# Kernel optimization log

Measured on AMD Instinct MI355X. Metric: run time of the kernel, lower is better.

## Reference

```python
import jax, jax.numpy as jnp
import numpy as np

N_NODES = 100000
N_EDGES = 1600000


def setup_inputs() -> dict:
    key = jax.random.key(0)
    ks = jax.random.split(key, 6)
    x = jax.random.normal(ks[0], (N_NODES, 128), dtype=jnp.float32)
    src = jax.random.randint(ks[1], (N_EDGES,), 0, N_NODES, dtype=jnp.int32)
    dst = jax.random.randint(ks[2], (N_EDGES,), 0, N_NODES, dtype=jnp.int32)
    # Glorot-ish scaled weights
    W1 = jax.random.normal(ks[3], (128, 64), dtype=jnp.float32) / np.sqrt(128.0)
    b1 = jnp.zeros((64,), dtype=jnp.float32)
    W2 = jax.random.normal(ks[4], (64, 64), dtype=jnp.float32) / np.sqrt(64.0)
    b2 = jnp.zeros((64,), dtype=jnp.float32)
    return {"x": x, "src": src, "dst": dst, "W1": W1, "b1": b1, "W2": W2, "b2": b2}


def _gcn_forward(x, src_f, dst_f, norm_src, norm_dst, W1, b1, W2, b2):
    n = x.shape[0]

    def conv(h, W, b):
        # weight-first (in_feats >= out_feats in DGL GraphConv): h W is cheap, aggregate small dim
        h = h @ W                                  # [N, d_out]
        h = h * norm_src[:, None]                  # D_out^{-1/2} on source side
        msg = h[src_f]                             # gather per edge [E+N, d_out]
        agg = jax.ops.segment_sum(msg, dst_f, num_segments=n)  # scatter-add to dst
        return agg * norm_dst[:, None] + b         # D_in^{-1/2} + bias

    h = jax.nn.relu(conv(x, W1, b1))
    return conv(h, W2, b2)


def reference(x, src, dst, W1, b1, W2, b2):
    n = x.shape[0]
    loop = jnp.arange(n, dtype=src.dtype)
    src_f = jnp.concatenate([src, loop])  # dgl.add_self_loop
    dst_f = jnp.concatenate([dst, loop])
    ones = jnp.ones(src_f.shape[0], dtype=x.dtype)
    out_deg = jax.ops.segment_sum(ones, src_f, num_segments=n)
    in_deg = jax.ops.segment_sum(ones, dst_f, num_segments=n)
    norm_src = jax.lax.rsqrt(out_deg)  # deg >= 1 due to self loops
    norm_dst = jax.lax.rsqrt(in_deg)
    return _gcn_forward(x, src_f, dst_f, norm_src, norm_dst, W1, b1, W2, b2)
```

## Files before the change

### kernel.cpp

```cpp
#include <hip/hip_runtime.h>
#include <hip/hip_fp16.h>

#define D 64
#define SLICE 33400
#define NBUCK 512
#define EPB 4096

typedef __attribute__((ext_vector_type(8))) short short8;
typedef __attribute__((ext_vector_type(4))) float floatx4;

__global__ __launch_bounds__(1024) void k_hist(const int* __restrict__ src,
                                               const int* __restrict__ dst,
                                               int* __restrict__ cnt_out,
                                               int* __restrict__ cnt_in,
                                               int E, int N) {
    __shared__ int h[SLICE];
    const int* idx = blockIdx.z ? dst : src;
    int* cnt       = blockIdx.z ? cnt_in : cnt_out;
    int lo = blockIdx.y * SLICE;
    int hi = min(lo + SLICE, N);
    int len = hi - lo;
    for (int i = threadIdx.x; i < len; i += 1024) h[i] = 0;
    __syncthreads();

    const int E4 = E >> 2;
    const int4* idx4 = (const int4*)idx;
    int stride = gridDim.x * 1024;
    for (int i = blockIdx.x * 1024 + threadIdx.x; i < E4; i += stride) {
        int4 v = idx4[i];
        if (v.x >= lo && v.x < hi) atomicAdd(&h[v.x - lo], 1);
        if (v.y >= lo && v.y < hi) atomicAdd(&h[v.y - lo], 1);
        if (v.z >= lo && v.z < hi) atomicAdd(&h[v.z - lo], 1);
        if (v.w >= lo && v.w < hi) atomicAdd(&h[v.w - lo], 1);
    }
    if (blockIdx.x == 0) {
        int e = E4 * 4 + threadIdx.x;
        if (e < E) {
            int v = idx[e];
            if (v >= lo && v < hi) atomicAdd(&h[v - lo], 1);
        }
    }
    __syncthreads();
    for (int i = threadIdx.x; i < len; i += 1024) {
        int c = h[i];
        if (c) atomicAdd(&cnt[lo + i], c);
    }
}

__global__ __launch_bounds__(256) void k_norm(const int* __restrict__ cnt,
                                              float* __restrict__ nrm, int n) {
    int i = blockIdx.x * 256 + threadIdx.x;
    if (i < n) nrm[i] = rsqrtf((float)cnt[i] + 1.0f);
}

__global__ __launch_bounds__(256) void k_scan1(const int* __restrict__ in,
                                               int* __restrict__ out,
                                               int* __restrict__ partials, int n) {
    __shared__ int s[256];
    int tid = threadIdx.x;
    int base = blockIdx.x * 1024 + tid * 4;
    int v[4];
#pragma unroll
    for (int j = 0; j < 4; ++j) v[j] = (base + j < n) ? in[base + j] : 0;
    int l1 = v[0] + v[1];
    int l2 = l1 + v[2];
    int total = l2 + v[3];
    s[tid] = total;
    __syncthreads();
    for (int off = 1; off < 256; off <<= 1) {
        int add = (tid >= off) ? s[tid - off] : 0;
        __syncthreads();
        s[tid] += add;
        __syncthreads();
    }
    int excl = s[tid] - total;
    if (base + 0 < n) out[base + 0] = excl;
    if (base + 1 < n) out[base + 1] = excl + v[0];
    if (base + 2 < n) out[base + 2] = excl + l1;
    if (base + 3 < n) out[base + 3] = excl + l2;
    if (tid == 255) partials[blockIdx.x] = s[255];
}

__global__ __launch_bounds__(256) void k_scan2(int* __restrict__ partials, int B,
                                               int* __restrict__ row_ptr, int N, int E) {
    __shared__ int s[256];
    int tid = threadIdx.x;
    int v = (tid < B) ? partials[tid] : 0;
    s[tid] = v;
    __syncthreads();
    for (int off = 1; off < 256; off <<= 1) {
        int add = (tid >= off) ? s[tid - off] : 0;
        __syncthreads();
        s[tid] += add;
        __syncthreads();
    }
    if (tid < B) partials[tid] = s[tid] - v;
    if (tid == 0) row_ptr[N] = E;
}

__global__ __launch_bounds__(256) void k_scan3(int* __restrict__ out,
                                               const int* __restrict__ partials, int n) {
    int off = partials[blockIdx.x];
    int base = blockIdx.x * 1024 + threadIdx.x * 4;
#pragma unroll
    for (int j = 0; j < 4; ++j)
        if (base + j < n) out[base + j] += off;
}

__global__ __launch_bounds__(256) void k_bin(const int* __restrict__ src,
                                             const int* __restrict__ dst,
                                             const int* __restrict__ row_ptr,
                                             int* __restrict__ bucket_cursor,
                                             unsigned long long* __restrict__ binned,
                                             int E) {
    __shared__ int cnt[NBUCK];
    __shared__ int bloc[NBUCK];
    __shared__ int lcur[NBUCK];
    __shared__ int gbase[NBUCK];
    __shared__ int ss[256];
    __shared__ unsigned long long stage[EPB];

    int tid = threadIdx.x;
    int start = blockIdx.x * EPB;
    int nloc = min(EPB, E - start);

    for (int i = tid; i < NBUCK; i += 256) cnt[i] = 0;
    __syncthreads();

#pragma unroll
    for (int r = 0; r < EPB / 256; ++r) {
        int idx = start + r * 256 + tid;
        if (idx < E) atomicAdd(&cnt[dst[idx] >> 8], 1);
    }
    __syncthreads();

    int a = cnt[2 * tid], b = cnt[2 * tid + 1];
    ss[tid] = a + b;
    __syncthreads();
    for (int off = 1; off < 256; off <<= 1) {
        int add = (tid >= off) ? ss[tid - off] : 0;
        __syncthreads();
        ss[tid] += add;
        __syncthreads();
    }
    int excl = ss[tid] - (a + b);
    bloc[2 * tid] = excl;           lcur[2 * tid] = excl;
    bloc[2 * tid + 1] = excl + a;   lcur[2 * tid + 1] = excl + a;
    __syncthreads();

    for (int bk = tid; bk < NBUCK; bk += 256) {
        int c = cnt[bk];
        gbase[bk] = c ? (atomicAdd(&bucket_cursor[bk], c) + row_ptr[bk << 8]) : 0;
    }
    __syncthreads();

#pragma unroll
    for (int r = 0; r < EPB / 256; ++r) {
        int idx = start + r * 256 + tid;
        if (idx < E) {
            int d = dst[idx];
            int p = atomicAdd(&lcur[d >> 8], 1);
            stage[p] = ((unsigned long long)(unsigned)d << 32) | (unsigned)src[idx];
        }
    }
    __syncthreads();

#pragma unroll
    for (int r = 0; r < EPB / 256; ++r) {
        int i = r * 256 + tid;
        if (i < nloc) {
            unsigned long long e = stage[i];
            int bk = (int)(e >> 40);
            binned[gbase[bk] + (i - bloc[bk])] = e;
        }
    }
}

__global__ __launch_bounds__(256) void k_bsort(const unsigned long long* __restrict__ binned,
                                               const int* __restrict__ row_ptr,
                                               int* __restrict__ csr, int N) {
    __shared__ int cur[256];
    int b = blockIdx.x;
    int n0 = b << 8;
    int tid = threadIdx.x;
    if (n0 + tid < N) cur[tid] = row_ptr[n0 + tid];
    __syncthreads();
    int base = row_ptr[n0];
    int c = row_ptr[min(n0 + 256, N)] - base;
    for (int k = tid; k < c; k += 256) {
        unsigned long long e = binned[base + k];
        int d = (int)(e >> 32);
        int s = (int)(e & 0xffffffffu);
        int p = atomicAdd(&cur[d - n0], 1);
        csr[p] = s;
    }
}

template <int K>
__global__ __launch_bounds__(256) void k_gemm_mfma(const float* __restrict__ hsrc,
                                                   const float* __restrict__ W,
                                                   const float* __restrict__ norm_src,
                                                   __half* __restrict__ t, int N) {
    constexpr int NKI = K / 32;
    __shared__ short Whi[NKI * 2048];
    __shared__ short Wlo[NKI * 2048];
    int tid = threadIdx.x;

    for (int f = tid; f < K * 64; f += 256) {
        int n  = f & 15;
        int j  = (f >> 4) & 7;
        int q  = (f >> 7) & 3;
        int ct = (f >> 9) & 3;
        int ki = f >> 11;
        int k = ki * 32 + q * 8 + j;
        int c = ct * 16 + n;
        float w = W[k * 64 + c];
        unsigned u = __float_as_uint(w);
        float l = w - __uint_as_float(u & 0xffff0000u);
        int idx = (((ki * 4 + ct) * 16 + n) * 4 + q) * 8 + j;
        Whi[idx] = (short)(u >> 16);
        Wlo[idx] = (short)(__float_as_uint(l) >> 16);
    }
    __syncthreads();

    int wave = tid >> 6, lane = tid & 63;
    int q = lane >> 4, n = lane & 15;
    int r0 = blockIdx.x * 64 + wave * 16;
    int rowc = min(r0 + n, N - 1);

    floatx4 acc[4] = {{0.f,0.f,0.f,0.f},{0.f,0.f,0.f,0.f},
                      {0.f,0.f,0.f,0.f},{0.f,0.f,0.f,0.f}};

    for (int ki = 0; ki < NKI; ++ki) {
        const float* ap = hsrc + (long long)rowc * K + ki * 32 + q * 8;
        float4 a0 = *(const float4*)ap;
        float4 a1 = *(const float4*)(ap + 4);
        float av[8] = {a0.x, a0.y, a0.z, a0.w, a1.x, a1.y, a1.z, a1.w};
        short8 ahi, alo;
#pragma unroll
        for (int j = 0; j < 8; ++j) {
            unsigned u = __float_as_uint(av[j]);
            float l = av[j] - __uint_as_float(u & 0xffff0000u);
            ahi[j] = (short)(u >> 16);
            alo[j] = (short)(__float_as_uint(l) >> 16);
        }
#pragma unroll
        for (int ct = 0; ct < 4; ++ct) {
            int bidx = (((ki * 4 + ct) * 16 + n) * 4 + q) * 8;
            short8 bhi = *(const short8*)&Whi[bidx];
            short8 blo = *(const short8*)&Wlo[bidx];
            acc[ct] = __builtin_amdgcn_mfma_f32_16x16x32_bf16(ahi, bhi, acc[ct], 0, 0, 0);
            acc[ct] = __builtin_amdgcn_mfma_f32_16x16x32_bf16(ahi, blo, acc[ct], 0, 0, 0);
            acc[ct] = __builtin_amdgcn_mfma_f32_16x16x32_bf16(alo, bhi, acc[ct], 0, 0, 0);
        }
    }

#pragma unroll
    for (int reg = 0; reg < 4; ++reg) {
        int orow = r0 + q * 4 + reg;
        if (orow < N) {
            float nrm = norm_src[orow];
#pragma unroll
            for (int ct = 0; ct < 4; ++ct)
                t[(long long)orow * 64 + ct * 16 + n] = __float2half(acc[ct][reg] * nrm);
        }
    }
}

__global__ __launch_bounds__(256) void k_agg(const int* __restrict__ row_ptr,
                                             const int* __restrict__ cnt,
                                             const int* __restrict__ csr,
                                             const __half* __restrict__ t,
                                             const float* __restrict__ norm_dst,
                                             const float* __restrict__ bias,
                                             float* __restrict__ out, int N, int do_relu) {
    int tid = threadIdx.x;
    int half_id = tid >> 5;
    int lane = tid & 31;
    int i = blockIdx.x * 8 + half_id;
    if (i >= N) return;
    const __half2* t2 = (const __half2*)t;
    int start = row_ptr[i], c = cnt[i];

    float2 sf = __half22float2(t2[i * 32 + lane]);
    float ax = sf.x, ay = sf.y;

    int j = 0;
    int pre = min(c, (4 - (start & 3)) & 3);
    for (; j < pre; ++j) {
        float2 f = __half22float2(t2[csr[start + j] * 32 + lane]);
        ax += f.x; ay += f.y;
    }
    for (; j + 8 <= c; j += 8) {
        int4 s4 = *(const int4*)&csr[start + j];
        int4 s5 = *(const int4*)&csr[start + j + 4];
        float2 f0 = __half22float2(t2[s4.x * 32 + lane]);
        float2 f1 = __half22float2(t2[s4.y * 32 + lane]);
        float2 f2 = __half22float2(t2[s4.z * 32 + lane]);
        float2 f3 = __half22float2(t2[s4.w * 32 + lane]);
        float2 f4 = __half22float2(t2[s5.x * 32 + lane]);
        float2 f5 = __half22float2(t2[s5.y * 32 + lane]);
        float2 f6 = __half22float2(t2[s5.z * 32 + lane]);
        float2 f7 = __half22float2(t2[s5.w * 32 + lane]);
        ax += ((f0.x + f1.x) + (f2.x + f3.x)) + ((f4.x + f5.x) + (f6.x + f7.x));
        ay += ((f0.y + f1.y) + (f2.y + f3.y)) + ((f4.y + f5.y) + (f6.y + f7.y));
    }
    for (; j + 4 <= c; j += 4) {
        int4 s4 = *(const int4*)&csr[start + j];
        float2 f0 = __half22float2(t2[s4.x * 32 + lane]);
        float2 f1 = __half22float2(t2[s4.y * 32 + lane]);
        float2 f2 = __half22float2(t2[s4.z * 32 + lane]);
        float2 f3 = __half22float2(t2[s4.w * 32 + lane]);
        ax += (f0.x + f1.x) + (f2.x + f3.x);
        ay += (f0.y + f1.y) + (f2.y + f3.y);
    }
    for (; j < c; ++j) {
        float2 f = __half22float2(t2[csr[start + j] * 32 + lane]);
        ax += f.x; ay += f.y;
    }

    float nrm = norm_dst[i];
    float2 bb = ((const float2*)bias)[lane];
    float vx = fmaf(ax, nrm, bb.x);
    float vy = fmaf(ay, nrm, bb.y);
    if (do_relu) { vx = fmaxf(vx, 0.f); vy = fmaxf(vy, 0.f); }
    float2 o; o.x = vx; o.y = vy;
    ((float2*)out)[i * 32 + lane] = o;
}

extern "C" void kernel_launch(void* const* d_in, const int* in_sizes, int n_in,
                              void* d_out, int out_size, void* d_ws, size_t ws_size,
                              hipStream_t stream) {
    const float* x   = (const float*)d_in[0];
    const int*   src = (const int*)d_in[1];
    const int*   dst = (const int*)d_in[2];
    const float* W1  = (const float*)d_in[3];
    const float* b1  = (const float*)d_in[4];
    const float* W2  = (const float*)d_in[5];
    const float* b2  = (const float*)d_in[6];
    float* out = (float*)d_out;

    const int N = in_sizes[0] / 128;
    const int E = in_sizes[1];

    int*   cnt_out  = (int*)d_ws;
    int*   cnt_in   = cnt_out + N;
    int*   row_ptr  = cnt_in + N;
    int*   partials = row_ptr + N + 1;
    float* norm_src = (float*)(partials + 1024);
    float* norm_dst = norm_src + N;
    long long toff = (5LL * N + 1025 + 63) & ~63LL;
    float* tbase    = (float*)d_ws + toff;
    float* h        = tbase + (long long)N * D;
    int*   csr      = (int*)(h + (long long)N * D);
    int*   bucket_cursor = csr + E;
    __half* t_h = (__half*)tbase;
    unsigned long long* binned = (unsigned long long*)tbase;

    const int B = (N + 1023) / 1024;
    const int NS = (N + SLICE - 1) / SLICE;
    const int NB = (N + 255) / 256;
    const int NBK = (E + EPB - 1) / EPB;

    hipMemsetAsync(cnt_out, 0, (size_t)2 * N * sizeof(int), stream);
    hipMemsetAsync(bucket_cursor, 0, (size_t)NBUCK * sizeof(int), stream);

    k_hist<<<dim3(42, NS, 2), 1024, 0, stream>>>(src, dst, cnt_out, cnt_in, E, N);
    k_norm<<<(2 * N + 255) / 256, 256, 0, stream>>>(cnt_out, norm_src, 2 * N);

    k_scan1<<<B, 256, 0, stream>>>(cnt_in, row_ptr, partials, N);
    k_scan2<<<1, 256, 0, stream>>>(partials, B, row_ptr, N, E);
    k_scan3<<<B, 256, 0, stream>>>(row_ptr, partials, N);

    k_bin<<<NBK, 256, 0, stream>>>(src, dst, row_ptr, bucket_cursor, binned, E);
    k_bsort<<<NB, 256, 0, stream>>>(binned, row_ptr, csr, N);

    k_gemm_mfma<128><<<(N + 63) / 64, 256, 0, stream>>>(x, W1, norm_src, t_h, N);
    k_agg<<<(N + 7) / 8, 256, 0, stream>>>(row_ptr, cnt_in, csr, t_h, norm_dst, b1, h, N, 1);

    k_gemm_mfma<64><<<(N + 63) / 64, 256, 0, stream>>>(h, W2, norm_src, t_h, N);
    k_agg<<<(N + 7) / 8, 256, 0, stream>>>(row_ptr, cnt_in, csr, t_h, norm_dst, b2, out, N, 0);
}
```

Baseline: 303.8 us.

## Derive CSR row pointers per bucket inside bsort instead of global in-degree scan

The per-node in-degree histogram and the three-kernel global scan are replaced by a 512-entry coarse bucket histogram folded into k_hist and a single-block bucket scan. Each k_bsort block now counts its own destination nodes, scans them locally, and writes row_ptr and both normalisation vectors, which removes k_norm and two scan kernels. This cuts kernel launches and a full pass over dst at node granularity, in exchange for an extra read of the binned edges inside k_bsort. k_agg now derives the degree from row_ptr differences.

```diff
diff --git a/kernel.cpp b/kernel.cpp
--- a/kernel.cpp
+++ b/kernel.cpp
@@ -12,22 +12,44 @@
 __global__ __launch_bounds__(1024) void k_hist(const int* __restrict__ src,
                                                const int* __restrict__ dst,
                                                int* __restrict__ cnt_out,
-                                               int* __restrict__ cnt_in,
+                                               int* __restrict__ bucket_cnt,
                                                int E, int N) {
     __shared__ int h[SLICE];
-    const int* idx = blockIdx.z ? dst : src;
-    int* cnt       = blockIdx.z ? cnt_in : cnt_out;
+    const int E4 = E >> 2;
+    int stride = gridDim.x * 1024;
+
+    if (blockIdx.y == gridDim.y - 1) {
+        for (int i = threadIdx.x; i < NBUCK; i += 1024) h[i] = 0;
+        __syncthreads();
+        const int4* d4 = (const int4*)dst;
+        for (int i = blockIdx.x * 1024 + threadIdx.x; i < E4; i += stride) {
+            int4 v = d4[i];
+            atomicAdd(&h[v.x >> 8], 1);
+            atomicAdd(&h[v.y >> 8], 1);
+            atomicAdd(&h[v.z >> 8], 1);
+            atomicAdd(&h[v.w >> 8], 1);
+        }
+        if (blockIdx.x == 0) {
+            int e = E4 * 4 + threadIdx.x;
+            if (e < E) atomicAdd(&h[dst[e] >> 8], 1);
+        }
+        __syncthreads();
+        for (int i = threadIdx.x; i < NBUCK; i += 1024) {
+            int c = h[i];
+            if (c) atomicAdd(&bucket_cnt[i], c);
+        }
+        return;
+    }
+
     int lo = blockIdx.y * SLICE;
     int hi = min(lo + SLICE, N);
     int len = hi - lo;
     for (int i = threadIdx.x; i < len; i += 1024) h[i] = 0;
     __syncthreads();
 
-    const int E4 = E >> 2;
-    const int4* idx4 = (const int4*)idx;
-    int stride = gridDim.x * 1024;
+    const int4* s4 = (const int4*)src;
     for (int i = blockIdx.x * 1024 + threadIdx.x; i < E4; i += stride) {
-        int4 v = idx4[i];
+        int4 v = s4[i];
         if (v.x >= lo && v.x < hi) atomicAdd(&h[v.x - lo], 1);
         if (v.y >= lo && v.y < hi) atomicAdd(&h[v.y - lo], 1);
         if (v.z >= lo && v.z < hi) atomicAdd(&h[v.z - lo], 1);
@@ -36,80 +58,39 @@
     if (blockIdx.x == 0) {
         int e = E4 * 4 + threadIdx.x;
         if (e < E) {
-            int v = idx[e];
+            int v = src[e];
             if (v >= lo && v < hi) atomicAdd(&h[v - lo], 1);
         }
     }
     __syncthreads();
     for (int i = threadIdx.x; i < len; i += 1024) {
         int c = h[i];
-        if (c) atomicAdd(&cnt[lo + i], c);
-    }
-}
-
-__global__ __launch_bounds__(256) void k_norm(const int* __restrict__ cnt,
-                                              float* __restrict__ nrm, int n) {
-    int i = blockIdx.x * 256 + threadIdx.x;
-    if (i < n) nrm[i] = rsqrtf((float)cnt[i] + 1.0f);
-}
-
-__global__ __launch_bounds__(256) void k_scan1(const int* __restrict__ in,
-                                               int* __restrict__ out,
-                                               int* __restrict__ partials, int n) {
-    __shared__ int s[256];
-    int tid = threadIdx.x;
-    int base = blockIdx.x * 1024 + tid * 4;
-    int v[4];
-#pragma unroll
-    for (int j = 0; j < 4; ++j) v[j] = (base + j < n) ? in[base + j] : 0;
-    int l1 = v[0] + v[1];
-    int l2 = l1 + v[2];
-    int total = l2 + v[3];
-    s[tid] = total;
-    __syncthreads();
-    for (int off = 1; off < 256; off <<= 1) {
+        if (c) atomicAdd(&cnt_out[lo + i], c);
+    }
+}
+
+__global__ __launch_bounds__(512) void k_scanB(const int* __restrict__ bucket_cnt,
+                                               int* __restrict__ bucket_ptr,
+                                               int* __restrict__ row_ptr, int N, int E) {
+    __shared__ int s[512];
+    int tid = threadIdx.x;
+    int v = bucket_cnt[tid];
+    s[tid] = v;
+    __syncthreads();
+    for (int off = 1; off < 512; off <<= 1) {
         int add = (tid >= off) ? s[tid - off] : 0;
         __syncthreads();
         s[tid] += add;
         __syncthreads();
     }
-    int excl = s[tid] - total;
-    if (base + 0 < n) out[base + 0] = excl;
-    if (base + 1 < n) out[base + 1] = excl + v[0];
-    if (base + 2 < n) out[base + 2] = excl + l1;
-    if (base + 3 < n) out[base + 3] = excl + l2;
-    if (tid == 255) partials[blockIdx.x] = s[255];
-}
-
-__global__ __launch_bounds__(256) void k_scan2(int* __restrict__ partials, int B,
-                                               int* __restrict__ row_ptr, int N, int E) {
-    __shared__ int s[256];
-    int tid = threadIdx.x;
-    int v = (tid < B) ? partials[tid] : 0;
-    s[tid] = v;
-    __syncthreads();
-    for (int off = 1; off < 256; off <<= 1) {
-        int add = (tid >= off) ? s[tid - off] : 0;
-        __syncthreads();
-        s[tid] += add;
-        __syncthreads();
-    }
-    if (tid < B) partials[tid] = s[tid] - v;
+    bucket_ptr[tid] = s[tid] - v;
+    if (tid == 511) bucket_ptr[512] = s[511];
     if (tid == 0) row_ptr[N] = E;
-}
-
-__global__ __launch_bounds__(256) void k_scan3(int* __restrict__ out,
-                                               const int* __restrict__ partials, int n) {
-    int off = partials[blockIdx.x];
-    int base = blockIdx.x * 1024 + threadIdx.x * 4;
-#pragma unroll
-    for (int j = 0; j < 4; ++j)
-        if (base + j < n) out[base + j] += off;
 }
 
 __global__ __launch_bounds__(256) void k_bin(const int* __restrict__ src,
                                              const int* __restrict__ dst,
-                                             const int* __restrict__ row_ptr,
+                                             const int* __restrict__ bucket_ptr,
                                              int* __restrict__ bucket_cursor,
                                              unsigned long long* __restrict__ binned,
                                              int E) {
@@ -150,7 +131,7 @@
 
     for (int bk = tid; bk < NBUCK; bk += 256) {
         int c = cnt[bk];
-        gbase[bk] = c ? (atomicAdd(&bucket_cursor[bk], c) + row_ptr[bk << 8]) : 0;
+        gbase[bk] = c ? (atomicAdd(&bucket_cursor[bk], c) + bucket_ptr[bk]) : 0;
     }
     __syncthreads();
 
@@ -177,22 +158,53 @@
 }
 
 __global__ __launch_bounds__(256) void k_bsort(const unsigned long long* __restrict__ binned,
-                                               const int* __restrict__ row_ptr,
-                                               int* __restrict__ csr, int N) {
+                                               const int* __restrict__ bucket_ptr,
+                                               const int* __restrict__ cnt_out,
+                                               int* __restrict__ csr,
+                                               int* __restrict__ row_ptr,
+                                               float* __restrict__ norm_src,
+                                               float* __restrict__ norm_dst, int N) {
+    __shared__ int cnt256[256];
+    __shared__ int ss[256];
     __shared__ int cur[256];
     int b = blockIdx.x;
     int n0 = b << 8;
     int tid = threadIdx.x;
-    if (n0 + tid < N) cur[tid] = row_ptr[n0 + tid];
-    __syncthreads();
-    int base = row_ptr[n0];
-    int c = row_ptr[min(n0 + 256, N)] - base;
-    for (int k = tid; k < c; k += 256) {
+    int base = bucket_ptr[b];
+    int ctot = bucket_ptr[b + 1] - base;
+
+    cnt256[tid] = 0;
+    __syncthreads();
+    for (int k = tid; k < ctot; k += 256) {
+        int d = (int)(binned[base + k] >> 32);
+        atomicAdd(&cnt256[d - n0], 1);
+    }
+    __syncthreads();
+
+    int v = cnt256[tid];
+    ss[tid] = v;
+    __syncthreads();
+    for (int off = 1; off < 256; off <<= 1) {
+        int add = (tid >= off) ? ss[tid - off] : 0;
+        __syncthreads();
+        ss[tid] += add;
+        __syncthreads();
+    }
+    int excl = ss[tid] - v;
+    int node = n0 + tid;
+    if (node < N) {
+        row_ptr[node] = base + excl;
+        norm_dst[node] = rsqrtf((float)v + 1.0f);
+        norm_src[node] = rsqrtf((float)cnt_out[node] + 1.0f);
+    }
+    cur[tid] = base + excl;
+    __syncthreads();
+
+    for (int k = tid; k < ctot; k += 256) {
         unsigned long long e = binned[base + k];
         int d = (int)(e >> 32);
-        int s = (int)(e & 0xffffffffu);
         int p = atomicAdd(&cur[d - n0], 1);
-        csr[p] = s;
+        csr[p] = (int)(e & 0xffffffffu);
     }
 }
 
@@ -268,7 +280,6 @@
 }
 
 __global__ __launch_bounds__(256) void k_agg(const int* __restrict__ row_ptr,
-                                             const int* __restrict__ cnt,
                                              const int* __restrict__ csr,
                                              const __half* __restrict__ t,
                                              const float* __restrict__ norm_dst,
@@ -280,7 +291,8 @@
     int i = blockIdx.x * 8 + half_id;
     if (i >= N) return;
     const __half2* t2 = (const __half2*)t;
-    int start = row_ptr[i], c = cnt[i];
+    int start = row_ptr[i];
+    int c = row_ptr[i + 1] - start;
 
     float2 sf = __half22float2(t2[i * 32 + lane]);
     float ax = sf.x, ay = sf.y;
@@ -343,41 +355,35 @@
     const int N = in_sizes[0] / 128;
     const int E = in_sizes[1];
 
-    int*   cnt_out  = (int*)d_ws;
-    int*   cnt_in   = cnt_out + N;
-    int*   row_ptr  = cnt_in + N;
-    int*   partials = row_ptr + N + 1;
-    float* norm_src = (float*)(partials + 1024);
-    float* norm_dst = norm_src + N;
-    long long toff = (5LL * N + 1025 + 63) & ~63LL;
+    int*   cnt_out       = (int*)d_ws;
+    int*   bucket_cnt    = cnt_out + N;
+    int*   bucket_cursor = bucket_cnt + 512;
+    int*   bucket_ptr    = bucket_cursor + 512;
+    int*   row_ptr       = bucket_ptr + 513;
+    float* norm_src      = (float*)(row_ptr + N + 1);
+    float* norm_dst      = norm_src + N;
+    long long toff = (4LL * N + 2562 + 63) & ~63LL;
     float* tbase    = (float*)d_ws + toff;
     float* h        = tbase + (long long)N * D;
     int*   csr      = (int*)(h + (long long)N * D);
-    int*   bucket_cursor = csr + E;
     __half* t_h = (__half*)tbase;
     unsigned long long* binned = (unsigned long long*)tbase;
 
-    const int B = (N + 1023) / 1024;
     const int NS = (N + SLICE - 1) / SLICE;
     const int NB = (N + 255) / 256;
     const int NBK = (E + EPB - 1) / EPB;
 
-    hipMemsetAsync(cnt_out, 0, (size_t)2 * N * sizeof(int), stream);
-    hipMemsetAsync(bucket_cursor, 0, (size_t)NBUCK * sizeof(int), stream);
-
-    k_hist<<<dim3(42, NS, 2), 1024, 0, stream>>>(src, dst, cnt_out, cnt_in, E, N);
-    k_norm<<<(2 * N + 255) / 256, 256, 0, stream>>>(cnt_out, norm_src, 2 * N);
-
-    k_scan1<<<B, 256, 0, stream>>>(cnt_in, row_ptr, partials, N);
-    k_scan2<<<1, 256, 0, stream>>>(partials, B, row_ptr, N, E);
-    k_scan3<<<B, 256, 0, stream>>>(row_ptr, partials, N);
-
-    k_bin<<<NBK, 256, 0, stream>>>(src, dst, row_ptr, bucket_cursor, binned, E);
-    k_bsort<<<NB, 256, 0, stream>>>(binned, row_ptr, csr, N);
+    hipMemsetAsync(cnt_out, 0, (size_t)(N + 1024) * sizeof(int), stream);
+
+    k_hist<<<dim3(42, NS + 1), 1024, 0, stream>>>(src, dst, cnt_out, bucket_cnt, E, N);
+    k_scanB<<<1, 512, 0, stream>>>(bucket_cnt, bucket_ptr, row_ptr, N, E);
+    k_bin<<<NBK, 256, 0, stream>>>(src, dst, bucket_ptr, bucket_cursor, binned, E);
+    k_bsort<<<NB, 256, 0, stream>>>(binned, bucket_ptr, cnt_out, csr, row_ptr,
+                                    norm_src, norm_dst, N);
 
     k_gemm_mfma<128><<<(N + 63) / 64, 256, 0, stream>>>(x, W1, norm_src, t_h, N);
-    k_agg<<<(N + 7) / 8, 256, 0, stream>>>(row_ptr, cnt_in, csr, t_h, norm_dst, b1, h, N, 1);
+    k_agg<<<(N + 7) / 8, 256, 0, stream>>>(row_ptr, csr, t_h, norm_dst, b1, h, N, 1);
 
     k_gemm_mfma<64><<<(N + 63) / 64, 256, 0, stream>>>(h, W2, norm_src, t_h, N);
-    k_agg<<<(N + 7) / 8, 256, 0, stream>>>(row_ptr, cnt_in, csr, t_h, norm_dst, b2, out, N, 0);
-}
+    k_agg<<<(N + 7) / 8, 256, 0, stream>>>(row_ptr, csr, t_h, norm_dst, b2, out, N, 0);
+}
```

Result: faster. 285.3 us (-6.1%).
